# Kernel tuning notes

Measured on AMD Instinct MI355X. Metric: run time of the kernel, lower is better.

Reference implementation:

```python
import jax, jax.numpy as jnp
import numpy as np

H = 2048
NUM_K = 16
NUM_V = 32
DK = 128
DV = 128
KSZ = 4
KEY_DIM = NUM_K * DK      # 2048
VALUE_DIM = NUM_V * DV    # 4096
CONV_DIM = 2 * KEY_DIM + VALUE_DIM  # 8192
EPS = 1e-6
VPK = NUM_V // NUM_K      # 2


def _l2norm(x, eps=1e-6):
    return x * jax.lax.rsqrt(jnp.sum(x * x, axis=-1, keepdims=True) + eps)


def setup_inputs() -> dict:
    key = jax.random.key(0)
    ks = jax.random.split(key, 12)
    s = 0.02
    return {
        "hidden_in": jax.random.normal(ks[0], (1, 1, H), jnp.float32),
        "conv_state": jax.random.normal(ks[1], (1, CONV_DIM, KSZ), jnp.float32),
        "rec_state": jax.random.normal(ks[2], (1, NUM_V, DK, DV), jnp.float32) * 0.1,
        "conv_w": jax.random.normal(ks[3], (CONV_DIM, KSZ), jnp.float32) * s,
        "in_proj_qkv_w": jax.random.normal(ks[4], (CONV_DIM, H), jnp.float32) * s,
        "in_proj_z_w": jax.random.normal(ks[5], (VALUE_DIM, H), jnp.float32) * s,
        "in_proj_b_w": jax.random.normal(ks[6], (NUM_V, H), jnp.float32) * s,
        "in_proj_a_w": jax.random.normal(ks[7], (NUM_V, H), jnp.float32) * s,
        "out_proj_w": jax.random.normal(ks[8], (H, VALUE_DIM), jnp.float32) * s,
        "dt_bias": jax.random.normal(ks[9], (NUM_V,), jnp.float32) * 0.1,
        "A_log": jax.random.normal(ks[10], (NUM_V,), jnp.float32) * 0.1,
        "norm_w": jnp.ones((DV,), jnp.float32),
    }


def reference(hidden_in, conv_state, rec_state, conv_w, in_proj_qkv_w,
              in_proj_z_w, in_proj_b_w, in_proj_a_w, out_proj_w,
              dt_bias, A_log, norm_w):
    # ---- projections (B=1, T=1) ----
    h = hidden_in[:, 0, :]                                   # (1, H)
    mixed_qkv = jnp.einsum('bh,ch->bc', h, in_proj_qkv_w)    # (1, CONV_DIM)
    z = jnp.einsum('bh,vh->bv', h, in_proj_z_w)              # (1, VALUE_DIM)
    b = jnp.einsum('bh,nh->bn', h, in_proj_b_w)              # (1, NUM_V)
    a = jnp.einsum('bh,nh->bn', h, in_proj_a_w)              # (1, NUM_V)

    # ---- causal conv1d update (shift state, append new token) ----
    w = jnp.concatenate([conv_state, mixed_qkv[:, :, None]], axis=-1)  # (1, C, K+1)
    new_conv_state = w[:, :, 1:]                                       # (1, C, K)
    conv_out = jax.nn.silu(jnp.sum(new_conv_state * conv_w[None], axis=-1))  # (1, C)

    # ---- split heads ----
    q = conv_out[:, :KEY_DIM].reshape(1, NUM_K, DK)
    k = conv_out[:, KEY_DIM:2 * KEY_DIM].reshape(1, NUM_K, DK)
    v = conv_out[:, 2 * KEY_DIM:].reshape(1, NUM_V, DV)
    # repeat_interleave key heads to match value heads (GQA-style)
    q = jnp.repeat(q, VPK, axis=1)                           # (1, NUM_V, DK)
    k = jnp.repeat(k, VPK, axis=1)

    q_ = _l2norm(q) * (1.0 / np.sqrt(DK))
    k_ = _l2norm(k)

    # ---- gating ----
    beta = jax.nn.sigmoid(b)                                  # (1, NUM_V)
    g = -jnp.exp(A_log) * jax.nn.softplus(a + dt_bias)        # (1, NUM_V)
    g_exp = jnp.exp(g)

    # ---- gated delta-rule recurrent update ----
    rec = rec_state * g_exp[:, :, None, None]                 # (1, NUM_V, DK, DV)
    kv_mem = jnp.einsum('bhkv,bhk->bhv', rec, k_)             # (1, NUM_V, DV)
    delta = (v - kv_mem) * beta[:, :, None]
    rec = rec + k_[:, :, :, None] * delta[:, :, None, :]
    core = jnp.einsum('bhkv,bhk->bhv', rec, q_)               # (1, NUM_V, DV)

    # ---- gated RMSNorm per value head ----
    x = core.reshape(-1, DV)
    zf = z.reshape(-1, DV)
    var = jnp.mean(x * x, axis=-1, keepdims=True)
    xn = (x * jax.lax.rsqrt(var + EPS)) * norm_w
    out = xn * jax.nn.silu(zf)                                # (NUM_V, DV)

    hidden_out = jnp.einsum('bv,hv->bh', out.reshape(1, VALUE_DIM), out_proj_w)
    hidden_out = hidden_out.reshape(1, 1, H)
    return hidden_out, new_conv_state, rec
```

## Files before the change

### kernel.cpp

```cpp
#include <hip/hip_runtime.h>
#include <math.h>

#define H_DIM 2048
#define NUM_K 16
#define NUM_V 32
#define DK 128
#define DV 128
#define KSZ 4
#define KEY_DIM 2048
#define VALUE_DIM 4096
#define CONV_DIM 8192

#define WS_QKV   0
#define WS_Z     8192
#define WS_B     12288
#define WS_A     12320
#define WS_CONV  12352
#define WS_OUT   20544

__device__ __forceinline__ float wave_reduce_sum(float v) {
#pragma unroll
    for (int off = 32; off > 0; off >>= 1) v += __shfl_down(v, off, 64);
    return v;
}

__global__ void proj_kernel(const float* __restrict__ h,
                            const float* __restrict__ qkv_w,
                            const float* __restrict__ z_w,
                            const float* __restrict__ b_w,
                            const float* __restrict__ a_w,
                            float* __restrict__ ws) {
    const int R = CONV_DIM + VALUE_DIM + 2 * NUM_V;
    int wave = (blockIdx.x * blockDim.x + threadIdx.x) >> 6;
    int lane = threadIdx.x & 63;
    if (wave >= R) return;

    const float* row;
    float* dst;
    if (wave < CONV_DIM) {
        row = qkv_w + (size_t)wave * H_DIM;
        dst = ws + WS_QKV + wave;
    } else if (wave < CONV_DIM + VALUE_DIM) {
        int r = wave - CONV_DIM;
        row = z_w + (size_t)r * H_DIM;
        dst = ws + WS_Z + r;
    } else if (wave < CONV_DIM + VALUE_DIM + NUM_V) {
        int r = wave - CONV_DIM - VALUE_DIM;
        row = b_w + (size_t)r * H_DIM;
        dst = ws + WS_B + r;
    } else {
        int r = wave - CONV_DIM - VALUE_DIM - NUM_V;
        row = a_w + (size_t)r * H_DIM;
        dst = ws + WS_A + r;
    }

    const float4* row4 = (const float4*)row;
    const float4* h4 = (const float4*)h;
    float acc = 0.f;
#pragma unroll
    for (int i = 0; i < H_DIM / 256; ++i) {
        float4 w4 = row4[lane + 64 * i];
        float4 hv = h4[lane + 64 * i];
        acc += w4.x * hv.x + w4.y * hv.y + w4.z * hv.z + w4.w * hv.w;
    }
    acc = wave_reduce_sum(acc);
    if (lane == 0) *dst = acc;
}

__global__ void conv_kernel_rw(const float* __restrict__ conv_state,
                               const float* __restrict__ conv_w,
                               float* __restrict__ ws,
                               float* __restrict__ new_conv_state) {
    int c = blockIdx.x * blockDim.x + threadIdx.x;
    if (c >= CONV_DIM) return;
    float4 cs = ((const float4*)conv_state)[c];
    float4 w = ((const float4*)conv_w)[c];
    float mq = ws[WS_QKV + c];
    float pre = cs.y * w.x + cs.z * w.y + cs.w * w.z + mq * w.w;
    float so = pre / (1.f + expf(-pre));
    ws[WS_CONV + c] = so;
    float4 ns;
    ns.x = cs.y; ns.y = cs.z; ns.z = cs.w; ns.w = mq;
    ((float4*)new_conv_state)[c] = ns;
}

__global__ void head_kernel(float* __restrict__ ws,
                            const float* __restrict__ rec_in,
                            const float* __restrict__ dt_bias,
                            const float* __restrict__ A_log,
                            const float* __restrict__ norm_w,
                            float* __restrict__ rec_out) {
    __shared__ float k_lds[DK];
    __shared__ float q_lds[DK];
    __shared__ float redk[2], redq[2], redc[2];

    int n = blockIdx.x;
    int v = threadIdx.x;
    int sh = n >> 1;
    int wid = v >> 6, lane = v & 63;

    const float* conv_out = ws + WS_CONV;
    float qraw = conv_out[sh * DK + v];
    float kraw = conv_out[KEY_DIM + sh * DK + v];
    float vval = conv_out[2 * KEY_DIM + n * DV + v];

    float ks = wave_reduce_sum(kraw * kraw);
    float qs = wave_reduce_sum(qraw * qraw);
    if (lane == 0) { redk[wid] = ks; redq[wid] = qs; }
    __syncthreads();
    float kin = rsqrtf(redk[0] + redk[1] + 1e-6f);
    float qin = rsqrtf(redq[0] + redq[1] + 1e-6f) * 0.08838834764831845f;
    k_lds[v] = kraw * kin;
    q_lds[v] = qraw * qin;

    float bb = ws[WS_B + n];
    float aa = ws[WS_A + n];
    float beta = 1.f / (1.f + expf(-bb));
    float x = aa + dt_bias[n];
    float sp = (x > 20.f) ? x : log1pf(expf(x));
    float gexp = expf(-expf(A_log[n]) * sp);
    __syncthreads();

    const float* rn = rec_in + (size_t)n * DK * DV;
    float* ro = rec_out + (size_t)n * DK * DV;

    float kv = 0.f;
#pragma unroll 8
    for (int k = 0; k < DK; ++k) kv += rn[k * DV + v] * k_lds[k];
    kv *= gexp;
    float delta = (vval - kv) * beta;

    float core = 0.f;
#pragma unroll 8
    for (int k = 0; k < DK; ++k) {
        float val = rn[k * DV + v] * gexp + k_lds[k] * delta;
        ro[k * DV + v] = val;
        core += val * q_lds[k];
    }

    float cs = wave_reduce_sum(core * core);
    if (lane == 0) redc[wid] = cs;
    __syncthreads();
    float var = (redc[0] + redc[1]) * (1.f / DV);
    float xn = core * rsqrtf(var + 1e-6f) * norm_w[v];
    float zv = ws[WS_Z + n * DV + v];
    float silz = zv / (1.f + expf(-zv));
    ws[WS_OUT + n * DV + v] = xn * silz;
}

__global__ void outproj_kernel(const float* __restrict__ ws,
                               const float* __restrict__ out_proj_w,
                               float* __restrict__ hidden_out) {
    int wave = (blockIdx.x * blockDim.x + threadIdx.x) >> 6;
    int lane = threadIdx.x & 63;
    if (wave >= H_DIM) return;
    const float4* row4 = (const float4*)(out_proj_w + (size_t)wave * VALUE_DIM);
    const float4* o4 = (const float4*)(ws + WS_OUT);
    float acc = 0.f;
#pragma unroll
    for (int i = 0; i < VALUE_DIM / 256; ++i) {
        float4 w4 = row4[lane + 64 * i];
        float4 ov = o4[lane + 64 * i];
        acc += w4.x * ov.x + w4.y * ov.y + w4.z * ov.z + w4.w * ov.w;
    }
    acc = wave_reduce_sum(acc);
    if (lane == 0) hidden_out[wave] = acc;
}

extern "C" void kernel_launch(void* const* d_in, const int* in_sizes, int n_in,
                              void* d_out, int out_size, void* d_ws, size_t ws_size,
                              hipStream_t stream) {
    const float* h          = (const float*)d_in[0];
    const float* conv_state = (const float*)d_in[1];
    const float* rec_in     = (const float*)d_in[2];
    const float* conv_w     = (const float*)d_in[3];
    const float* qkv_w      = (const float*)d_in[4];
    const float* z_w        = (const float*)d_in[5];
    const float* b_w        = (const float*)d_in[6];
    const float* a_w        = (const float*)d_in[7];
    const float* out_proj_w = (const float*)d_in[8];
    const float* dt_bias    = (const float*)d_in[9];
    const float* A_log      = (const float*)d_in[10];
    const float* norm_w     = (const float*)d_in[11];

    float* out = (float*)d_out;
    float* hidden_out = out;
    float* new_conv   = out + H_DIM;
    float* rec_out    = out + H_DIM + CONV_DIM * KSZ;
    float* ws = (float*)d_ws;

    proj_kernel<<<3088, 256, 0, stream>>>(h, qkv_w, z_w, b_w, a_w, ws);
    conv_kernel_rw<<<32, 256, 0, stream>>>(conv_state, conv_w, ws, new_conv);
    head_kernel<<<32, 128, 0, stream>>>(ws, rec_in, dt_bias, A_log, norm_w, rec_out);
    outproj_kernel<<<512, 256, 0, stream>>>(ws, out_proj_w, hidden_out);
}
```

Measured before the change: 40.28 us.

## Fuse conv update into head kernel and widen recurrent update with float4 split-K

The separate conv1d kernel is removed. Each head block now computes the q, k and v conv outputs it needs and writes the new conv state, sharing them through LDS. This saves a launch and the round trip of conv outputs through the workspace. The head kernel also moves from 128 to 512 threads. Each thread handles a float4 column group over an 8-row chunk of the recurrent state, and partial sums are reduced through shared memory, to raise memory-level parallelism on the 2 MB state read and write. The cost is extra barriers and some duplicated q/k conv work and state writes across paired heads.

New measurement: 32.81 us. 18.6% less time.

```diff
diff --git a/kernel.cpp b/kernel.cpp
--- a/kernel.cpp
+++ b/kernel.cpp
@@ -15,7 +15,6 @@
 #define WS_Z     8192
 #define WS_B     12288
 #define WS_A     12320
-#define WS_CONV  12352
 #define WS_OUT   20544
 
 __device__ __forceinline__ float wave_reduce_sum(float v) {
@@ -67,51 +66,67 @@
     if (lane == 0) *dst = acc;
 }
 
-__global__ void conv_kernel_rw(const float* __restrict__ conv_state,
-                               const float* __restrict__ conv_w,
-                               float* __restrict__ ws,
-                               float* __restrict__ new_conv_state) {
-    int c = blockIdx.x * blockDim.x + threadIdx.x;
-    if (c >= CONV_DIM) return;
-    float4 cs = ((const float4*)conv_state)[c];
-    float4 w = ((const float4*)conv_w)[c];
-    float mq = ws[WS_QKV + c];
-    float pre = cs.y * w.x + cs.z * w.y + cs.w * w.z + mq * w.w;
-    float so = pre / (1.f + expf(-pre));
-    ws[WS_CONV + c] = so;
-    float4 ns;
-    ns.x = cs.y; ns.y = cs.z; ns.z = cs.w; ns.w = mq;
-    ((float4*)new_conv_state)[c] = ns;
-}
-
-__global__ void head_kernel(float* __restrict__ ws,
-                            const float* __restrict__ rec_in,
-                            const float* __restrict__ dt_bias,
-                            const float* __restrict__ A_log,
-                            const float* __restrict__ norm_w,
-                            float* __restrict__ rec_out) {
-    __shared__ float k_lds[DK];
-    __shared__ float q_lds[DK];
-    __shared__ float redk[2], redq[2], redc[2];
-
-    int n = blockIdx.x;
-    int v = threadIdx.x;
-    int sh = n >> 1;
-    int wid = v >> 6, lane = v & 63;
-
-    const float* conv_out = ws + WS_CONV;
-    float qraw = conv_out[sh * DK + v];
-    float kraw = conv_out[KEY_DIM + sh * DK + v];
-    float vval = conv_out[2 * KEY_DIM + n * DV + v];
-
-    float ks = wave_reduce_sum(kraw * kraw);
-    float qs = wave_reduce_sum(qraw * qraw);
-    if (lane == 0) { redk[wid] = ks; redq[wid] = qs; }
-    __syncthreads();
-    float kin = rsqrtf(redk[0] + redk[1] + 1e-6f);
-    float qin = rsqrtf(redq[0] + redq[1] + 1e-6f) * 0.08838834764831845f;
-    k_lds[v] = kraw * kin;
-    q_lds[v] = qraw * qin;
+__global__ __launch_bounds__(512) void head_kernel(
+        const float* __restrict__ conv_state,
+        const float* __restrict__ conv_w,
+        float* __restrict__ ws,
+        const float* __restrict__ rec_in,
+        const float* __restrict__ dt_bias,
+        const float* __restrict__ A_log,
+        const float* __restrict__ norm_w,
+        float* __restrict__ new_conv_state,
+        float* __restrict__ rec_out) {
+    __shared__ float qc[DK];
+    __shared__ float kc[DK];
+    __shared__ float vc[DV];
+    __shared__ float delta_lds[DV];
+    __shared__ float part[16][DV];
+    __shared__ float red[4];
+
+    const int n = blockIdx.x;
+    const int sh = n >> 1;
+    const int t = threadIdx.x;
+    const int lane = t & 63;
+
+    if (t < 384) {
+        int slice = t >> 7;
+        int j = t & 127;
+        int c;
+        if (slice == 0)      c = sh * DK + j;
+        else if (slice == 1) c = KEY_DIM + sh * DK + j;
+        else                 c = 2 * KEY_DIM + n * DV + j;
+        float4 cs = ((const float4*)conv_state)[c];
+        float4 w  = ((const float4*)conv_w)[c];
+        float mq  = ws[WS_QKV + c];
+        float pre = cs.y * w.x + cs.z * w.y + cs.w * w.z + mq * w.w;
+        float so  = pre / (1.f + expf(-pre));
+        if (slice == 0)      qc[j] = so;
+        else if (slice == 1) kc[j] = so;
+        else                 vc[j] = so;
+        float4 ns; ns.x = cs.y; ns.y = cs.z; ns.z = cs.w; ns.w = mq;
+        ((float4*)new_conv_state)[c] = ns;
+    }
+    __syncthreads();
+
+    if (t < 64) {
+        float s = qc[t] * qc[t] + qc[t + 64] * qc[t + 64];
+        s = wave_reduce_sum(s);
+        if (lane == 0) red[0] = s;
+    } else if (t < 128) {
+        int j = t - 64;
+        float s = kc[j] * kc[j] + kc[j + 64] * kc[j + 64];
+        s = wave_reduce_sum(s);
+        if (lane == 0) red[1] = s;
+    }
+    __syncthreads();
+    {
+        float qin = rsqrtf(red[0] + 1e-6f) * 0.08838834764831845f;
+        float kin = rsqrtf(red[1] + 1e-6f);
+        if (t < 128) {
+            qc[t] *= qin;
+            kc[t] *= kin;
+        }
+    }
 
     float bb = ws[WS_B + n];
     float aa = ws[WS_A + n];
@@ -121,31 +136,71 @@
     float gexp = expf(-expf(A_log[n]) * sp);
     __syncthreads();
 
-    const float* rn = rec_in + (size_t)n * DK * DV;
-    float* ro = rec_out + (size_t)n * DK * DV;
-
-    float kv = 0.f;
-#pragma unroll 8
-    for (int k = 0; k < DK; ++k) kv += rn[k * DV + v] * k_lds[k];
-    kv *= gexp;
-    float delta = (vval - kv) * beta;
-
-    float core = 0.f;
-#pragma unroll 8
-    for (int k = 0; k < DK; ++k) {
-        float val = rn[k * DV + v] * gexp + k_lds[k] * delta;
-        ro[k * DV + v] = val;
-        core += val * q_lds[k];
-    }
-
-    float cs = wave_reduce_sum(core * core);
-    if (lane == 0) redc[wid] = cs;
-    __syncthreads();
-    float var = (redc[0] + redc[1]) * (1.f / DV);
-    float xn = core * rsqrtf(var + 1e-6f) * norm_w[v];
-    float zv = ws[WS_Z + n * DV + v];
-    float silz = zv / (1.f + expf(-zv));
-    ws[WS_OUT + n * DV + v] = xn * silz;
+    const float4* rn4 = (const float4*)(rec_in + (size_t)n * DK * DV);
+    float4* ro4 = (float4*)(rec_out + (size_t)n * DK * DV);
+    const int cg = t & 31;
+    const int ch = t >> 5;
+
+    {
+        float4 kv = {0.f, 0.f, 0.f, 0.f};
+#pragma unroll
+        for (int j = 0; j < 8; ++j) {
+            int k = ch * 8 + j;
+            float4 r = rn4[k * 32 + cg];
+            float kk = kc[k];
+            kv.x += r.x * kk; kv.y += r.y * kk; kv.z += r.z * kk; kv.w += r.w * kk;
+        }
+        ((float4*)part[ch])[cg] = kv;
+    }
+    __syncthreads();
+    if (t < DV) {
+        float kv = 0.f;
+#pragma unroll
+        for (int c = 0; c < 16; ++c) kv += part[c][t];
+        kv *= gexp;
+        delta_lds[t] = (vc[t] - kv) * beta;
+    }
+    __syncthreads();
+
+    {
+        float4 d4 = ((const float4*)delta_lds)[cg];
+        float4 core = {0.f, 0.f, 0.f, 0.f};
+#pragma unroll
+        for (int j = 0; j < 8; ++j) {
+            int k = ch * 8 + j;
+            float4 r = rn4[k * 32 + cg];
+            float kk = kc[k];
+            float4 val;
+            val.x = r.x * gexp + kk * d4.x;
+            val.y = r.y * gexp + kk * d4.y;
+            val.z = r.z * gexp + kk * d4.z;
+            val.w = r.w * gexp + kk * d4.w;
+            ro4[k * 32 + cg] = val;
+            float qq = qc[k];
+            core.x += val.x * qq; core.y += val.y * qq;
+            core.z += val.z * qq; core.w += val.w * qq;
+        }
+        ((float4*)part[ch])[cg] = core;
+    }
+    __syncthreads();
+
+    if (t < DV) {
+        float core = 0.f;
+#pragma unroll
+        for (int c = 0; c < 16; ++c) core += part[c][t];
+        float s = wave_reduce_sum(core * core);
+        if (lane == 0) red[2 + (t >> 6)] = s;
+        vc[t] = core;
+    }
+    __syncthreads();
+    if (t < DV) {
+        float core = vc[t];
+        float var = (red[2] + red[3]) * (1.f / DV);
+        float xn = core * rsqrtf(var + 1e-6f) * norm_w[t];
+        float zv = ws[WS_Z + n * DV + t];
+        float silz = zv / (1.f + expf(-zv));
+        ws[WS_OUT + n * DV + t] = xn * silz;
+    }
 }
 
 __global__ void outproj_kernel(const float* __restrict__ ws,
@@ -190,7 +245,7 @@
     float* ws = (float*)d_ws;
 
     proj_kernel<<<3088, 256, 0, stream>>>(h, qkv_w, z_w, b_w, a_w, ws);
-    conv_kernel_rw<<<32, 256, 0, stream>>>(conv_state, conv_w, ws, new_conv);
-    head_kernel<<<32, 128, 0, stream>>>(ws, rec_in, dt_bias, A_log, norm_w, rec_out);
+    head_kernel<<<32, 512, 0, stream>>>(conv_state, conv_w, ws, rec_in,
+                                        dt_bias, A_log, norm_w, new_conv, rec_out);
     outproj_kernel<<<512, 256, 0, stream>>>(ws, out_proj_w, hidden_out);
 }
```
